# Performance work log

Measured on AMD Instinct MI355X. Metric: run time of the kernel, lower is better.

## Reference

```python
import jax, jax.numpy as jnp
import numpy as np

CHEB_K = 3  # from init_kwargs


def setup_inputs() -> dict:
    key = jax.random.key(0)
    k1, k2, k3, k4 = jax.random.split(key, 4)
    B, N, C_IN, C_OUT, D = 32, 4096, 32, 64, 16
    x = jax.random.normal(k1, (B, N, C_IN), dtype=jnp.float32)
    node_embeddings = jax.random.normal(k2, (N, D), dtype=jnp.float32)
    laplacian_mx = jnp.zeros((N, N), dtype=jnp.float32)  # unused by forward
    weights_pool = jax.random.normal(k3, (D, CHEB_K, C_IN, C_OUT), dtype=jnp.float32) * 0.1
    bias_pool = jax.random.normal(k4, (D, C_OUT), dtype=jnp.float32) * 0.1
    return {
        'x': x,
        'node_embeddings': node_embeddings,
        'laplacian_mx': laplacian_mx,
        'weights_pool': weights_pool,
        'bias_pool': bias_pool,
    }


def reference(x, node_embeddings, laplacian_mx, weights_pool, bias_pool):
    N = node_embeddings.shape[0]
    # adaptive adjacency: softmax(relu(E E^T)) over rows
    supports = jax.nn.softmax(jax.nn.relu(node_embeddings @ node_embeddings.T), axis=1)
    # Chebyshev recursion T_0=I, T_1=A, T_k = 2A T_{k-1} - T_{k-2}
    support_set = [jnp.eye(N, dtype=x.dtype), supports]
    for _ in range(2, CHEB_K):
        support_set.append(2.0 * supports @ support_set[-1] - support_set[-2])
    supports_k = jnp.stack(support_set, axis=0)  # [K, N, N]
    # per-node generated weights/bias
    weights = jnp.einsum('nd,dkio->nkio', node_embeddings, weights_pool)  # [N,K,I,O]
    bias = node_embeddings @ bias_pool  # [N, O]
    # graph propagation: [K,N,N] x [B,N,I] -> [B,K,N,I] -> [B,N,K,I]
    x_g = jnp.einsum('knm,bmc->bknc', supports_k, x).transpose(0, 2, 1, 3)
    # per-node grouped GEMM
    out = jnp.einsum('bnki,nkio->bno', x_g, weights) + bias
    return out
```

## Files before the change

kernel.cpp:

```cpp
#include <hip/hip_runtime.h>
#include <hip/hip_bf16.h>

#define N_NODES 4096
#define BATCH   32
#define CIN     32
#define COUT    64
#define DEMB    16
#define NCOL    (BATCH * CIN)
#define KIO     (3 * CIN * COUT)
#define SPLITK  4

typedef __bf16 bf16x8 __attribute__((ext_vector_type(8)));
typedef float  floatx4 __attribute__((ext_vector_type(4)));

__device__ inline void load_lds16(const void* g, void* l) {
    __builtin_amdgcn_global_load_lds(
        (const __attribute__((address_space(1))) void*)g,
        (__attribute__((address_space(3))) void*)l, 16, 0, 0);
}

__global__ __launch_bounds__(256) void compute_U_kernel(
        const float* __restrict__ E, __hip_bfloat16* __restrict__ U,
        float* __restrict__ invRow) {
    const int n0   = blockIdx.x * 8;
    const int t    = threadIdx.x;
    const int lane = t & 63, wave = t >> 6;
    __shared__ float red[4][8];

    float en[8][DEMB];
#pragma unroll
    for (int r = 0; r < 8; ++r) {
        const float4* er = (const float4*)&E[(size_t)(n0 + r) * DEMB];
        const float4 a0 = er[0], a1 = er[1], a2 = er[2], a3 = er[3];
        en[r][ 0]=a0.x; en[r][ 1]=a0.y; en[r][ 2]=a0.z; en[r][ 3]=a0.w;
        en[r][ 4]=a1.x; en[r][ 5]=a1.y; en[r][ 6]=a1.z; en[r][ 7]=a1.w;
        en[r][ 8]=a2.x; en[r][ 9]=a2.y; en[r][10]=a2.z; en[r][11]=a2.w;
        en[r][12]=a3.x; en[r][13]=a3.y; en[r][14]=a3.z; en[r][15]=a3.w;
    }

    float sum[8] = {0.f, 0.f, 0.f, 0.f, 0.f, 0.f, 0.f, 0.f};

    for (int tile = 0; tile < 16; ++tile) {
        const int c = tile * 256 + t;
        const float4* em4 = (const float4*)&E[(size_t)c * DEMB];
        const float4 b0 = em4[0], b1 = em4[1], b2 = em4[2], b3 = em4[3];
        float em[DEMB];
        em[ 0]=b0.x; em[ 1]=b0.y; em[ 2]=b0.z; em[ 3]=b0.w;
        em[ 4]=b1.x; em[ 5]=b1.y; em[ 6]=b1.z; em[ 7]=b1.w;
        em[ 8]=b2.x; em[ 9]=b2.y; em[10]=b2.z; em[11]=b2.w;
        em[12]=b3.x; em[13]=b3.y; em[14]=b3.z; em[15]=b3.w;
#pragma unroll
        for (int r = 0; r < 8; ++r) {
            float dt = 0.f;
#pragma unroll
            for (int d = 0; d < DEMB; ++d) dt += en[r][d] * em[d];
            const float ev = __expf(fmaxf(dt, 0.f));
            sum[r] += ev;
            U[(size_t)(n0 + r) * N_NODES + c] = __float2bfloat16(ev);
        }
    }
#pragma unroll
    for (int r = 0; r < 8; ++r)
#pragma unroll
        for (int off = 32; off > 0; off >>= 1) sum[r] += __shfl_xor(sum[r], off);
    if (lane == 0)
#pragma unroll
        for (int r = 0; r < 8; ++r) red[wave][r] = sum[r];
    __syncthreads();
    if (t < 8)
        invRow[n0 + t] = 1.0f / (red[0][t] + red[1][t] + red[2][t] + red[3][t]);
}

__global__ __launch_bounds__(256) void transpose_kernel(
        const float* __restrict__ x,
        __hip_bfloat16* __restrict__ Xt, __hip_bfloat16* __restrict__ Bt) {
    const int m0 = blockIdx.x * 64;
    const int b  = blockIdx.y;
    const int t  = threadIdx.x;
    __shared__ float tile[64][33];
    {
        const int ml = t >> 2, cg = (t & 3) * 8;
        const float* src = &x[((size_t)b * N_NODES + (m0 + ml)) * CIN + cg];
        const float4 r0 = *(const float4*)src;
        const float4 r1 = *(const float4*)(src + 4);
        tile[ml][cg+0] = r0.x; tile[ml][cg+1] = r0.y; tile[ml][cg+2] = r0.z; tile[ml][cg+3] = r0.w;
        tile[ml][cg+4] = r1.x; tile[ml][cg+5] = r1.y; tile[ml][cg+6] = r1.z; tile[ml][cg+7] = r1.w;
    }
    __syncthreads();
    {
        const int ml = t >> 2, cg = (t & 3) * 8;
        __hip_bfloat16* dst = &Xt[(size_t)(m0 + ml) * NCOL + b * CIN + cg];
#pragma unroll
        for (int j = 0; j < 8; ++j) dst[j] = __float2bfloat16(tile[ml][cg + j]);
    }
    {
        const int c = t >> 3, mg = (t & 7) * 8;
        __hip_bfloat16* dst = &Bt[(size_t)(b * CIN + c) * N_NODES + m0 + mg];
#pragma unroll
        for (int j = 0; j < 8; ++j) dst[j] = __float2bfloat16(tile[mg + j][c]);
    }
}

__global__ __launch_bounds__(256) void gen_w_kernel(
        const float* __restrict__ E, const float* __restrict__ Wp,
        __hip_bfloat16* __restrict__ Wn) {
    const int c   = blockIdx.x >> 3;
    const int oo0 = (blockIdx.x & 7) * 8;
    const int nc  = blockIdx.y * 64;
    const int t   = threadIdx.x;
    const int kk  = t & 31;
    const int oo  = oo0 + (t >> 5);

    __shared__ float et[64][DEMB];
    ((float4*)et)[t] = ((const float4*)&E[(size_t)nc * DEMB])[t];
    __syncthreads();

    const int srccol = (c * 32 + kk) * 64 + oo;
    float w[DEMB];
#pragma unroll
    for (int d = 0; d < DEMB; ++d) w[d] = Wp[(size_t)d * KIO + srccol];

    const int dstoff = c * 2048 + (oo >> 4) * 512 + (oo & 15) * 32 + kk;
    for (int nl = 0; nl < 64; ++nl) {
        float acc = 0.0f;
#pragma unroll
        for (int d = 0; d < DEMB; ++d) acc += et[nl][d] * w[d];
        Wn[(size_t)(nc + nl) * KIO + dstoff] = __float2bfloat16(acc);
    }
}

#define GBM 256
#define GBN 256
#define GBK 64

__global__ __launch_bounds__(512, 2) void gemm_splitk_kernel(
        const __hip_bfloat16* __restrict__ A,
        const __hip_bfloat16* __restrict__ Bt,
        __hip_bfloat16* __restrict__ P,
        int M, int NC, int K) {
    const int t    = threadIdx.x;
    const int row0 = blockIdx.x * GBM;
    const int col0 = blockIdx.y * GBN;
    const int z    = blockIdx.z;
    const int NT   = (K >> 6) / SPLITK;
    const int kb0  = z * NT * GBK;

    __shared__ alignas(16) __hip_bfloat16 As[2][16384];
    __shared__ alignas(16) __hip_bfloat16 Bs[2][16384];

    const int lane = t & 63, wave = t >> 6;
    const int l16 = lane & 15, quad = lane >> 4;
    const int wr = wave >> 2, wc = wave & 3;

    const int R0 = wr * 128 + l16;
    const int C0 = wc * 64 + l16;
    const int u_par = (l16 & 1) * 4 + quad;
    const int Aoff = (R0 >> 1) * 64 + ((u_par ^ ((R0 >> 1) & 7)) * 8);
    const int Boff = (C0 >> 1) * 64 + ((u_par ^ ((C0 >> 1) & 7)) * 8);

    auto stageA = [&](int buf, int kb, int kh, int s) {
        const int L = s * 512 + t;
        const int p = L >> 3, j = L & 7;
        const int u = j ^ (p & 7);
        const int rr = p * 2 + (u >> 2);
        const int qq = u & 3;
        load_lds16(&A[(size_t)(row0 + rr) * K + kb + kh * 32 + qq * 8],
                   &As[buf][(size_t)(kh * 1024 + L) * 8]);
    };
    auto stageB = [&](int buf, int kb, int kh, int s) {
        const int L = s * 512 + t;
        const int p = L >> 3, j = L & 7;
        const int u = j ^ (p & 7);
        const int rr = p * 2 + (u >> 2);
        const int qq = u & 3;
        load_lds16(&Bt[(size_t)(col0 + rr) * K + kb + kh * 32 + qq * 8],
                   &Bs[buf][(size_t)(kh * 1024 + L) * 8]);
    };

    floatx4 acc[8][4] = {};

#pragma unroll
    for (int s = 0; s < 2; ++s) stageA(0, kb0, 0, s);
#pragma unroll
    for (int s = 0; s < 2; ++s) stageB(0, kb0, 0, s);
#pragma unroll
    for (int s = 0; s < 2; ++s) stageA(0, kb0, 1, s);
#pragma unroll
    for (int s = 0; s < 2; ++s) stageB(0, kb0, 1, s);
#pragma unroll
    for (int s = 0; s < 2; ++s) stageA(1, kb0 + GBK, 0, s);
#pragma unroll
    for (int s = 0; s < 2; ++s) stageB(1, kb0 + GBK, 0, s);
    asm volatile("s_waitcnt vmcnt(4)" ::: "memory");
    __builtin_amdgcn_s_barrier();

    for (int tt = 0; tt < NT; ++tt) {
        const int buf = tt & 1;
        const int nb1 = buf ^ 1;
        const int nb2 = buf;
        const int kb1 = kb0 + (tt + 1) * GBK;
        const int kb2 = kb0 + (tt + 2) * GBK;
        const bool g1 = (tt + 1 < NT), g2 = (tt + 2 < NT);

        bf16x8 bfrag[4], afrag[4];

#pragma unroll
        for (int n = 0; n < 4; ++n)
            bfrag[n] = *(const bf16x8*)&Bs[buf][n * 512 + Boff];
#pragma unroll
        for (int m = 0; m < 4; ++m)
            afrag[m] = *(const bf16x8*)&As[buf][m * 512 + Aoff];
        if (g1) { stageA(nb1, kb1, 1, 0); stageA(nb1, kb1, 1, 1); }
        __builtin_amdgcn_s_barrier();
        __builtin_amdgcn_s_setprio(1);
#pragma unroll
        for (int m = 0; m < 4; ++m)
#pragma unroll
            for (int n = 0; n < 4; ++n)
                acc[m][n] = __builtin_amdgcn_mfma_f32_16x16x32_bf16(
                                afrag[m], bfrag[n], acc[m][n], 0, 0, 0);
        __builtin_amdgcn_s_setprio(0);
        __builtin_amdgcn_s_barrier();

#pragma unroll
        for (int m = 0; m < 4; ++m)
            afrag[m] = *(const bf16x8*)&As[buf][2048 + m * 512 + Aoff];
        if (g1) { stageB(nb1, kb1, 1, 0); stageB(nb1, kb1, 1, 1); }
        __builtin_amdgcn_s_barrier();
        __builtin_amdgcn_s_setprio(1);
#pragma unroll
        for (int m = 0; m < 4; ++m)
#pragma unroll
            for (int n = 0; n < 4; ++n)
                acc[4 + m][n] = __builtin_amdgcn_mfma_f32_16x16x32_bf16(
                                    afrag[m], bfrag[n], acc[4 + m][n], 0, 0, 0);
        __builtin_amdgcn_s_setprio(0);
        __builtin_amdgcn_s_barrier();

#pragma unroll
        for (int n = 0; n < 4; ++n)
            bfrag[n] = *(const bf16x8*)&Bs[buf][8192 + n * 512 + Boff];
#pragma unroll
        for (int m = 0; m < 4; ++m)
            afrag[m] = *(const bf16x8*)&As[buf][8192 + m * 512 + Aoff];
        if (g2) { stageA(nb2, kb2, 0, 0); stageA(nb2, kb2, 0, 1); }
        __builtin_amdgcn_s_barrier();
        __builtin_amdgcn_s_setprio(1);
#pragma unroll
        for (int m = 0; m < 4; ++m)
#pragma unroll
            for (int n = 0; n < 4; ++n)
                acc[m][n] = __builtin_amdgcn_mfma_f32_16x16x32_bf16(
                                afrag[m], bfrag[n], acc[m][n], 0, 0, 0);
        __builtin_amdgcn_s_setprio(0);
        __builtin_amdgcn_s_barrier();

#pragma unroll
        for (int m = 0; m < 4; ++m)
            afrag[m] = *(const bf16x8*)&As[buf][8192 + 2048 + m * 512 + Aoff];
        if (g2) { stageB(nb2, kb2, 0, 0); stageB(nb2, kb2, 0, 1); }
        __builtin_amdgcn_s_barrier();
        __builtin_amdgcn_s_setprio(1);
#pragma unroll
        for (int m = 0; m < 4; ++m)
#pragma unroll
            for (int n = 0; n < 4; ++n)
                acc[4 + m][n] = __builtin_amdgcn_mfma_f32_16x16x32_bf16(
                                    afrag[m], bfrag[n], acc[4 + m][n], 0, 0, 0);
        __builtin_amdgcn_s_setprio(0);
        if (tt < NT - 2) asm volatile("s_waitcnt vmcnt(4)" ::: "memory");
        else             asm volatile("s_waitcnt vmcnt(0)" ::: "memory");
        __builtin_amdgcn_s_barrier();
    }

    __hip_bfloat16* Pz = P + (size_t)z * M * NC;
#pragma unroll
    for (int mq = 0; mq < 2; ++mq)
#pragma unroll
        for (int m = 0; m < 4; ++m)
#pragma unroll
            for (int n = 0; n < 4; ++n)
#pragma unroll
                for (int r = 0; r < 4; ++r) {
                    const int rg = row0 + wr * 128 + mq * 64 + m * 16 + quad * 4 + r;
                    const int cg = col0 + wc * 64 + n * 16 + l16;
                    Pz[(size_t)rg * NC + cg] = __float2bfloat16(acc[mq * 4 + m][n][r]);
                }
}

__global__ __launch_bounds__(256) void combine1_kernel(
        const __hip_bfloat16* __restrict__ P, const float* __restrict__ invRow,
        __hip_bfloat16* __restrict__ Y, __hip_bfloat16* __restrict__ Yt,
        int M, int NC) {
    const int c0 = blockIdx.x * 64, m0 = blockIdx.y * 64;
    const int t = threadIdx.x;
    __shared__ float tile[64][65];
    const size_t stride = (size_t)M * NC;
#pragma unroll
    for (int j = 0; j < 16; ++j) {
        const int lin = t + j * 256;
        const int r = lin >> 6, c = lin & 63;
        const size_t idx = (size_t)(m0 + r) * NC + c0 + c;
        float s = 0.f;
#pragma unroll
        for (int z = 0; z < SPLITK; ++z) s += __bfloat162float(P[idx + z * stride]);
        s *= invRow[m0 + r];
        tile[r][c] = s;
        Y[idx] = __float2bfloat16(s);
    }
    __syncthreads();
#pragma unroll
    for (int j = 0; j < 16; ++j) {
        const int lin = t + j * 256;
        const int c = lin >> 6, r = lin & 63;
        Yt[(size_t)(c0 + c) * M + m0 + r] = __float2bfloat16(tile[r][c]);
    }
}

__global__ __launch_bounds__(256) void final_kernel(
        const __hip_bfloat16* __restrict__ Xt, const __hip_bfloat16* __restrict__ Y1,
        const __hip_bfloat16* __restrict__ P,  const float* __restrict__ invRow,
        const __hip_bfloat16* __restrict__ Wn,
        const float* __restrict__ E, const float* __restrict__ bias_pool,
        float* __restrict__ out) {
    const int t    = threadIdx.x;
    const int lane = t & 63, wave = t >> 6;
    const int l16  = lane & 15, quad = lane >> 4;
    const int n0   = blockIdx.x * 4;
    const int n    = n0 + wave;

    __shared__ float ost[32][4][65];

    const __hip_bfloat16* Wnode = Wn + (size_t)n * KIO;
    const float inv = invRow[n];
    const size_t pstride = (size_t)N_NODES * NCOL;

    floatx4 acc[2][4] = {};

    bf16x8 afX[2], afY1[2], afY2[2];
#pragma unroll
    for (int mt = 0; mt < 2; ++mt) {
        const size_t fo = (size_t)n * NCOL + (mt * 16 + l16) * 32 + quad * 8;
        afX[mt]  = *(const bf16x8*)&Xt[fo];
        afY1[mt] = *(const bf16x8*)&Y1[fo];
        const bf16x8 p0 = *(const bf16x8*)&P[fo];
        const bf16x8 p1 = *(const bf16x8*)&P[fo + pstride];
        const bf16x8 p2 = *(const bf16x8*)&P[fo + 2 * pstride];
        const bf16x8 p3 = *(const bf16x8*)&P[fo + 3 * pstride];
#pragma unroll
        for (int j = 0; j < 8; ++j) {
            const float s = (float)p0[j] + (float)p1[j] + (float)p2[j] + (float)p3[j];
            afY2[mt][j] = (__bf16)(2.0f * inv * s - (float)afX[mt][j]);
        }
    }

    const bf16x8* afs[3] = {afX, afY1, afY2};
#pragma unroll
    for (int c = 0; c < 3; ++c) {
#pragma unroll
        for (int ot = 0; ot < 4; ++ot) {
            const bf16x8 bfr = *(const bf16x8*)&Wnode[(size_t)c * 2048 +
                                                      ot * 512 + l16 * 32 + quad * 8];
#pragma unroll
            for (int mt = 0; mt < 2; ++mt)
                acc[mt][ot] = __builtin_amdgcn_mfma_f32_16x16x32_bf16(
                                  afs[c][mt], bfr, acc[mt][ot], 0, 0, 0);
        }
    }

    float en[DEMB];
#pragma unroll
    for (int d = 0; d < DEMB; ++d) en[d] = E[(size_t)n * DEMB + d];
#pragma unroll
    for (int ot = 0; ot < 4; ++ot) {
        float bv = 0.f;
        const int o = ot * 16 + l16;
#pragma unroll
        for (int d = 0; d < DEMB; ++d) bv += en[d] * bias_pool[d * COUT + o];
#pragma unroll
        for (int mt = 0; mt < 2; ++mt)
#pragma unroll
            for (int r = 0; r < 4; ++r) {
                const int b = mt * 16 + quad * 4 + r;
                ost[b][wave][o] = acc[mt][ot][r] + bv;
            }
    }
    __syncthreads();

#pragma unroll
    for (int j = 0; j < 8; ++j) {
        const int c  = t + j * 256;
        const int b  = c >> 6;
        const int rm = c & 63;
        const int nl = rm >> 4, o4 = (rm & 15) * 4;
        float4 v;
        v.x = ost[b][nl][o4 + 0]; v.y = ost[b][nl][o4 + 1];
        v.z = ost[b][nl][o4 + 2]; v.w = ost[b][nl][o4 + 3];
        *(float4*)&out[((size_t)b * N_NODES + n0 + nl) * COUT + o4] = v;
    }
}

extern "C" void kernel_launch(void* const* d_in, const int* in_sizes, int n_in,
                              void* d_out, int out_size, void* d_ws, size_t ws_size,
                              hipStream_t stream) {
    (void)in_sizes; (void)n_in; (void)out_size; (void)ws_size;
    const float* x  = (const float*)d_in[0];
    const float* E  = (const float*)d_in[1];
    const float* Wp = (const float*)d_in[3];
    const float* bp = (const float*)d_in[4];
    float* out = (float*)d_out;

    char* ws = (char*)d_ws;
    __hip_bfloat16* U    = (__hip_bfloat16*)(ws);
    __hip_bfloat16* Bt1  = (__hip_bfloat16*)(ws + 33554432);
    __hip_bfloat16* Y1t  = (__hip_bfloat16*)(ws + 41943040);
    __hip_bfloat16* P    = (__hip_bfloat16*)(ws + 50331648);
    __hip_bfloat16* Y1   = (__hip_bfloat16*)(ws + 83886080);
    __hip_bfloat16* Xt   = (__hip_bfloat16*)(ws + 92274688);
    float*       invRow  = (float*)(ws + 100663296);
    __hip_bfloat16* Wn   = (__hip_bfloat16*)(ws);

    compute_U_kernel<<<N_NODES / 8, 256, 0, stream>>>(E, U, invRow);
    transpose_kernel<<<dim3(N_NODES / 64, BATCH), 256, 0, stream>>>(x, Xt, Bt1);
    gemm_splitk_kernel<<<dim3(N_NODES / GBM, NCOL / GBN, SPLITK), 512, 0, stream>>>(
        U, Bt1, P, N_NODES, NCOL, N_NODES);
    combine1_kernel<<<dim3(NCOL / 64, N_NODES / 64), 256, 0, stream>>>(
        P, invRow, Y1, Y1t, N_NODES, NCOL);
    gemm_splitk_kernel<<<dim3(N_NODES / GBM, NCOL / GBN, SPLITK), 512, 0, stream>>>(
        U, Y1t, P, N_NODES, NCOL, N_NODES);
    gen_w_kernel<<<dim3(24, N_NODES / 64), 256, 0, stream>>>(E, Wp, Wn);
    final_kernel<<<N_NODES / 4, 256, 0, stream>>>(Xt, Y1, P, invRow, Wn, E, bp, out);
}
```

Before: 279.0 us.

## Use 128x128 split-K-2 GEMM for first propagation and pin schedule in second

```diff
diff --git a/kernel.cpp b/kernel.cpp
--- a/kernel.cpp
+++ b/kernel.cpp
@@ -8,7 +8,8 @@
 #define DEMB    16
 #define NCOL    (BATCH * CIN)
 #define KIO     (3 * CIN * COUT)
-#define SPLITK  4
+#define SK1     2
+#define SK2     4
 
 typedef __bf16 bf16x8 __attribute__((ext_vector_type(8)));
 typedef float  floatx4 __attribute__((ext_vector_type(4)));
@@ -129,11 +130,79 @@
     }
 }
 
+__global__ __launch_bounds__(256) void gemm128_kernel(
+        const __hip_bfloat16* __restrict__ A,
+        const __hip_bfloat16* __restrict__ Bt,
+        __hip_bfloat16* __restrict__ P,
+        int M, int NC, int K) {
+    const int t    = threadIdx.x;
+    const int row0 = blockIdx.x * 128;
+    const int col0 = blockIdx.y * 128;
+    const int z    = blockIdx.z;
+    const int iters = K >> 6;
+    const int q = iters / SK1, rem = iters % SK1;
+    const int it0 = z * q + (z < rem ? z : rem);
+    const int it1 = it0 + q + (z < rem ? 1 : 0);
+
+    __shared__ alignas(16) __hip_bfloat16 As[128 * 64];
+    __shared__ alignas(16) __hip_bfloat16 Bs[128 * 64];
+    const int lane = t & 63, wave = t >> 6;
+    const int l16 = lane & 15, quad = lane >> 4;
+    const int wrow = (wave >> 1) * 64, wcol = (wave & 1) * 64;
+    const int xr = l16 & 7;
+
+    floatx4 acc[4][4] = {};
+
+    for (int it = it0; it < it1; ++it) {
+        const int kb = it << 6;
+        __syncthreads();
+#pragma unroll
+        for (int s = 0; s < 4; ++s) {
+            const int gi = s * 256 + t;
+            const int r  = gi >> 3;
+            const int cg = (gi & 7) ^ (r & 7);
+            load_lds16(&A [(size_t)(row0 + r) * K + kb + cg * 8], &As[gi * 8]);
+            load_lds16(&Bt[(size_t)(col0 + r) * K + kb + cg * 8], &Bs[gi * 8]);
+        }
+        __syncthreads();
+#pragma unroll
+        for (int ks = 0; ks < 2; ++ks) {
+            bf16x8 af[4], bfr[4];
+#pragma unroll
+            for (int i = 0; i < 4; ++i)
+                af[i]  = *(const bf16x8*)&As[(wrow + i * 16 + l16) * 64 +
+                                             (((ks * 4 + quad) ^ xr) * 8)];
+#pragma unroll
+            for (int i = 0; i < 4; ++i)
+                bfr[i] = *(const bf16x8*)&Bs[(wcol + i * 16 + l16) * 64 +
+                                             (((ks * 4 + quad) ^ xr) * 8)];
+#pragma unroll
+            for (int i = 0; i < 4; ++i)
+#pragma unroll
+                for (int j = 0; j < 4; ++j)
+                    acc[i][j] = __builtin_amdgcn_mfma_f32_16x16x32_bf16(
+                                    af[i], bfr[j], acc[i][j], 0, 0, 0);
+        }
+    }
+
+    __hip_bfloat16* Pz = P + (size_t)z * M * NC;
+#pragma unroll
+    for (int i = 0; i < 4; ++i)
+#pragma unroll
+        for (int j = 0; j < 4; ++j)
+#pragma unroll
+            for (int r = 0; r < 4; ++r) {
+                const int rg = row0 + wrow + i * 16 + quad * 4 + r;
+                const int cg = col0 + wcol + j * 16 + l16;
+                Pz[(size_t)rg * NC + cg] = __float2bfloat16(acc[i][j][r]);
+            }
+}
+
 #define GBM 256
 #define GBN 256
 #define GBK 64
 
-__global__ __launch_bounds__(512, 2) void gemm_splitk_kernel(
+__global__ __launch_bounds__(512, 2) void gemm256_pinned_kernel(
         const __hip_bfloat16* __restrict__ A,
         const __hip_bfloat16* __restrict__ Bt,
         __hip_bfloat16* __restrict__ P,
@@ -142,7 +211,7 @@
     const int row0 = blockIdx.x * GBM;
     const int col0 = blockIdx.y * GBN;
     const int z    = blockIdx.z;
-    const int NT   = (K >> 6) / SPLITK;
+    const int NT   = (K >> 6) / SK2;
     const int kb0  = z * NT * GBK;
 
     __shared__ alignas(16) __hip_bfloat16 As[2][16384];
@@ -193,10 +262,11 @@
     for (int s = 0; s < 2; ++s) stageB(1, kb0 + GBK, 0, s);
     asm volatile("s_waitcnt vmcnt(4)" ::: "memory");
     __builtin_amdgcn_s_barrier();
+    __builtin_amdgcn_sched_barrier(0);
 
     for (int tt = 0; tt < NT; ++tt) {
         const int buf = tt & 1;
-        const int nb1 = buf ^ 1;
+        const int nb1 = (tt + 1) & 1;
         const int nb2 = buf;
         const int kb1 = kb0 + (tt + 1) * GBK;
         const int kb2 = kb0 + (tt + 2) * GBK;
@@ -212,6 +282,8 @@
             afrag[m] = *(const bf16x8*)&As[buf][m * 512 + Aoff];
         if (g1) { stageA(nb1, kb1, 1, 0); stageA(nb1, kb1, 1, 1); }
         __builtin_amdgcn_s_barrier();
+        asm volatile("s_waitcnt lgkmcnt(0)" ::: "memory");
+        __builtin_amdgcn_sched_barrier(0);
         __builtin_amdgcn_s_setprio(1);
 #pragma unroll
         for (int m = 0; m < 4; ++m)
@@ -227,6 +299,8 @@
             afrag[m] = *(const bf16x8*)&As[buf][2048 + m * 512 + Aoff];
         if (g1) { stageB(nb1, kb1, 1, 0); stageB(nb1, kb1, 1, 1); }
         __builtin_amdgcn_s_barrier();
+        asm volatile("s_waitcnt lgkmcnt(0)" ::: "memory");
+        __builtin_amdgcn_sched_barrier(0);
         __builtin_amdgcn_s_setprio(1);
 #pragma unroll
         for (int m = 0; m < 4; ++m)
@@ -245,6 +319,8 @@
             afrag[m] = *(const bf16x8*)&As[buf][8192 + m * 512 + Aoff];
         if (g2) { stageA(nb2, kb2, 0, 0); stageA(nb2, kb2, 0, 1); }
         __builtin_amdgcn_s_barrier();
+        asm volatile("s_waitcnt lgkmcnt(0)" ::: "memory");
+        __builtin_amdgcn_sched_barrier(0);
         __builtin_amdgcn_s_setprio(1);
 #pragma unroll
         for (int m = 0; m < 4; ++m)
@@ -260,6 +336,8 @@
             afrag[m] = *(const bf16x8*)&As[buf][8192 + 2048 + m * 512 + Aoff];
         if (g2) { stageB(nb2, kb2, 0, 0); stageB(nb2, kb2, 0, 1); }
         __builtin_amdgcn_s_barrier();
+        asm volatile("s_waitcnt lgkmcnt(0)" ::: "memory");
+        __builtin_amdgcn_sched_barrier(0);
         __builtin_amdgcn_s_setprio(1);
 #pragma unroll
         for (int m = 0; m < 4; ++m)
@@ -271,6 +349,7 @@
         if (tt < NT - 2) asm volatile("s_waitcnt vmcnt(4)" ::: "memory");
         else             asm volatile("s_waitcnt vmcnt(0)" ::: "memory");
         __builtin_amdgcn_s_barrier();
+        __builtin_amdgcn_sched_barrier(0);
     }
 
     __hip_bfloat16* Pz = P + (size_t)z * M * NC;
@@ -303,7 +382,7 @@
         const size_t idx = (size_t)(m0 + r) * NC + c0 + c;
         float s = 0.f;
 #pragma unroll
-        for (int z = 0; z < SPLITK; ++z) s += __bfloat162float(P[idx + z * stride]);
+        for (int z = 0; z < SK1; ++z) s += __bfloat162float(P[idx + z * stride]);
         s *= invRow[m0 + r];
         tile[r][c] = s;
         Y[idx] = __float2bfloat16(s);
@@ -422,11 +501,11 @@
 
     compute_U_kernel<<<N_NODES / 8, 256, 0, stream>>>(E, U, invRow);
     transpose_kernel<<<dim3(N_NODES / 64, BATCH), 256, 0, stream>>>(x, Xt, Bt1);
-    gemm_splitk_kernel<<<dim3(N_NODES / GBM, NCOL / GBN, SPLITK), 512, 0, stream>>>(
+    gemm128_kernel<<<dim3(N_NODES / 128, NCOL / 128, SK1), 256, 0, stream>>>(
         U, Bt1, P, N_NODES, NCOL, N_NODES);
     combine1_kernel<<<dim3(NCOL / 64, N_NODES / 64), 256, 0, stream>>>(
         P, invRow, Y1, Y1t, N_NODES, NCOL);
-    gemm_splitk_kernel<<<dim3(N_NODES / GBM, NCOL / GBN, SPLITK), 512, 0, stream>>>(
+    gemm256_pinned_kernel<<<dim3(N_NODES / GBM, NCOL / GBN, SK2), 512, 0, stream>>>(
         U, Y1t, P, N_NODES, NCOL, N_NODES);
     gen_w_kernel<<<dim3(24, N_NODES / 64), 256, 0, stream>>>(E, Wp, Wn);
     final_kernel<<<N_NODES / 4, 256, 0, stream>>>(Xt, Y1, P, invRow, Wn, E, bp, out);
```

After: 280.4 us. No clear change (+0.5%).
